# Performance work log

Measured on AMD Instinct MI355X. Metric: run time of the kernel, lower is better.

The kernel has to match this reference:

```python
import jax, jax.numpy as jnp
import numpy as np

S, HID = 2048, 4096
H, KV, D = 32, 8, 128
EPS = 1e-6
THETA = 10000.0


def setup_inputs() -> dict:
    key = jax.random.key(0)
    k0, k1, k2 = jax.random.split(key, 3)
    return {
        "positions": jnp.arange(S, dtype=jnp.int32),
        "hidden_states": jax.random.normal(k0, (S, HID), jnp.float32),
        "w_qkv": jax.random.normal(k1, ((H + 2 * KV) * D, HID), jnp.float32) * 0.02,
        "w_o": jax.random.normal(k2, (HID, H * D), jnp.float32) * 0.02,
        "gq": jnp.ones((D,), jnp.float32),
        "gk": jnp.ones((D,), jnp.float32),
    }


def _rmsnorm(x, g):
    # per-head RMSNorm over last dim (head_dim)
    return x * jax.lax.rsqrt(jnp.mean(x * x, axis=-1, keepdims=True) + EPS) * g


def _rope(x, positions):
    # NeoX-style rotary embedding, rotary_dim == head_dim
    half = D // 2
    inv_freq = 1.0 / (THETA ** (jnp.arange(half, dtype=jnp.float32) * 2.0 / D))
    freqs = positions.astype(jnp.float32)[:, None] * inv_freq  # [S, half]
    cos = jnp.cos(freqs)[:, None, :]  # [S, 1, half]
    sin = jnp.sin(freqs)[:, None, :]
    x1, x2 = x[..., :half], x[..., half:]
    return jnp.concatenate([x1 * cos - x2 * sin, x2 * cos + x1 * sin], axis=-1)


def reference(positions, hidden_states, w_qkv, w_o, gq, gk):
    qkv = hidden_states @ w_qkv.T  # [S, (H+2KV)*D]
    q = qkv[:, : H * D].reshape(S, H, D)
    k = qkv[:, H * D : (H + KV) * D].reshape(S, KV, D)
    v = qkv[:, (H + KV) * D :].reshape(S, KV, D)

    q = _rmsnorm(q, gq)
    k = _rmsnorm(k, gk)
    q = _rope(q, positions)
    k = _rope(k, positions)

    rep = H // KV
    kf = jnp.repeat(k, rep, axis=1)  # [S, H, D]
    vf = jnp.repeat(v, rep, axis=1)

    scale = D ** -0.5
    scores = jnp.einsum("qhd,khd->hqk", q, kf) * scale  # [H, S, S]
    causal = jnp.tril(jnp.ones((S, S), dtype=bool))
    scores = jnp.where(causal[None], scores, jnp.finfo(scores.dtype).min)
    attn = jax.nn.softmax(scores, axis=-1)
    ctx = jnp.einsum("hqk,khd->qhd", attn, vf).reshape(S, H * D)
    return ctx @ w_o.T  # [S, HID]
```

## Files before the change

kernel.cpp:

```cpp
#include <hip/hip_runtime.h>
#include <hip/hip_bf16.h>

#define S_LEN 2048
#define HID   4096
#define NH    32
#define NKV   8
#define DH    128
#define NQKV  ((NH + 2*NKV) * DH)

typedef __attribute__((ext_vector_type(8))) short s16x8;
typedef __attribute__((ext_vector_type(4))) short s16x4;
typedef __attribute__((ext_vector_type(4))) float f32x4;

__device__ __forceinline__ short f2bf(float x) {
    union { __hip_bfloat16 b; short s; } u;
    u.b = __float2bfloat16(x);
    return u.s;
}
__device__ __forceinline__ float bf2f(short s) {
    union { unsigned int u; float f; } v;
    v.u = ((unsigned int)(unsigned short)s) << 16;
    return v.f;
}

__device__ __forceinline__ void gload16(const void* g, void* l) {
    __builtin_amdgcn_global_load_lds(
        (const __attribute__((address_space(1))) void*)g,
        (__attribute__((address_space(3))) void*)l,
        16, 0, 0);
}

__device__ __forceinline__ void cstore(float* p, float v) { *p = v; }
__device__ __forceinline__ void cstore(short* p, float v) { *p = f2bf(v); }

__global__ __launch_bounds__(256) void convert_hs_wqkv(
        const float* __restrict__ in1, short* __restrict__ o1, long n1,
        const float* __restrict__ in2, short* __restrict__ o2, long n2)
{
    const long total = n1 + n2;
    long i0 = ((long)blockIdx.x * blockDim.x + threadIdx.x) * 4;
    long stride = (long)gridDim.x * blockDim.x * 4;
    for (long i = i0; i < total; i += stride) {
        const float* src; short* dst; long off;
        if (i < n1) { src = in1; dst = o1; off = i; }
        else        { src = in2; dst = o2; off = i - n1; }
        float4 v = *(const float4*)(src + off);
        s16x4 o;
        o[0] = f2bf(v.x); o[1] = f2bf(v.y); o[2] = f2bf(v.z); o[3] = f2bf(v.w);
        *(s16x4*)(dst + off) = o;
    }
}

template <typename OT>
__global__ __launch_bounds__(512, 2) void gemm192(
        const short* __restrict__ A, const short* __restrict__ B,
        OT* __restrict__ C, int M, int N, int K)
{
    __shared__ char lds[114688];
    const int t = threadIdx.x;
    const int w = t >> 6, l = t & 63, g = l >> 4, q16 = l & 15;
    const int wm = w >> 2, wn = w & 3;
    const int bx = blockIdx.x, by = blockIdx.y;
    const int NT = K >> 6;

    const int r0 = t >> 3, c0 = t & 7;
    const int scA = c0 ^ (r0 & 7);
    const long KB64  = (long)K * 128;
    const long KB128 = (long)K * 256;
    const long gA00 = ((long)(by * 256 + r0) * K) * 2 + scA * 16;
    long gBoff[3];
#pragma unroll
    for (int i = 0; i < 3; ++i) {
        int row = (i * 512 + t) >> 3;
        int chunk = (t & 7) ^ (row & 7);
        gBoff[i] = ((long)(bx * 192 + row) * K) * 2 + chunk * 16;
    }
    const int dstw = w * 1024;

    auto SA = [&](int kt, int h) {
        char* d = lds + ((kt & 1) * 2 + h) * 16384 + dstw;
        const long s0 = gA00 + h * KB128 + (long)kt * 128;
        gload16((const char*)A + s0, d);
        gload16((const char*)A + s0 + KB64, d + 8192);
    };
    auto SB = [&](int kt) {
        char* d = lds + 65536 + (kt & 1) * 24576 + dstw;
        const long kb = (long)kt * 128;
#pragma unroll
        for (int i = 0; i < 3; ++i)
            gload16((const char*)B + gBoff[i] + kb, d + i * 8192);
    };

    const int arow = q16 * 128;
    const int brow = (wn * 48 + q16) * 128;
    const int sw0 = ((g) ^ (q16 & 7)) << 4;
    const int sw1 = ((4 + g) ^ (q16 & 7)) << 4;

    f32x4 acc[8][3] = {};
    s16x8 a0f[4][2], a1f[4][2], b0f[2][2], b1f[2];

    SB(0); SA(0, 0); SA(0, 1);
    SB(1); SA(1, 0); SA(1, 1);
    asm volatile("s_waitcnt vmcnt(7)" ::: "memory");
    __builtin_amdgcn_s_barrier();

    for (int kt = 0; kt < NT; ++kt) {
        const int b = kt & 1;
        const char* As_ = lds + (b * 2 + wm) * 16384;
        const char* Bs_ = lds + 65536 + b * 24576;

#pragma unroll
        for (int mi = 0; mi < 4; ++mi) {
            a0f[mi][0] = *(const s16x8*)(As_ + arow + mi*2048 + sw0);
            a0f[mi][1] = *(const s16x8*)(As_ + arow + mi*2048 + sw1);
        }
#pragma unroll
        for (int ni = 0; ni < 2; ++ni) {
            b0f[ni][0] = *(const s16x8*)(Bs_ + brow + ni*2048 + sw0);
            b0f[ni][1] = *(const s16x8*)(Bs_ + brow + ni*2048 + sw1);
        }
        __builtin_amdgcn_s_barrier();
        asm volatile("s_waitcnt lgkmcnt(0)" ::: "memory");
        __builtin_amdgcn_sched_barrier(0);
        __builtin_amdgcn_s_setprio(1);
#pragma unroll
        for (int mi = 0; mi < 4; ++mi)
#pragma unroll
            for (int ni = 0; ni < 2; ++ni)
#pragma unroll
                for (int kk = 0; kk < 2; ++kk)
                    acc[mi][ni] = __builtin_amdgcn_mfma_f32_16x16x32_bf16(
                            a0f[mi][kk], b0f[ni][kk], acc[mi][ni], 0, 0, 0);
        __builtin_amdgcn_s_setprio(0);
        __builtin_amdgcn_s_barrier();

        b1f[0] = *(const s16x8*)(Bs_ + brow + 2*2048 + sw0);
        b1f[1] = *(const s16x8*)(Bs_ + brow + 2*2048 + sw1);
#pragma unroll
        for (int mi = 0; mi < 4; ++mi) {
            a1f[mi][0] = *(const s16x8*)(As_ + arow + 8192 + mi*2048 + sw0);
            a1f[mi][1] = *(const s16x8*)(As_ + arow + 8192 + mi*2048 + sw1);
        }
        __builtin_amdgcn_s_barrier();
        asm volatile("s_waitcnt lgkmcnt(0)" ::: "memory");
        __builtin_amdgcn_sched_barrier(0);
        __builtin_amdgcn_s_setprio(1);
#pragma unroll
        for (int mi = 0; mi < 4; ++mi)
#pragma unroll
            for (int kk = 0; kk < 2; ++kk)
                acc[mi][2] = __builtin_amdgcn_mfma_f32_16x16x32_bf16(
                        a0f[mi][kk], b1f[kk], acc[mi][2], 0, 0, 0);
#pragma unroll
        for (int mi = 0; mi < 4; ++mi)
#pragma unroll
            for (int kk = 0; kk < 2; ++kk)
                acc[4+mi][2] = __builtin_amdgcn_mfma_f32_16x16x32_bf16(
                        a1f[mi][kk], b1f[kk], acc[4+mi][2], 0, 0, 0);
        __builtin_amdgcn_s_setprio(0);
        __builtin_amdgcn_s_barrier();

        if (kt + 2 < NT) { SB(kt + 2); SA(kt + 2, 0); SA(kt + 2, 1); }
        __builtin_amdgcn_s_setprio(1);
#pragma unroll
        for (int mi = 0; mi < 4; ++mi)
#pragma unroll
            for (int ni = 0; ni < 2; ++ni)
#pragma unroll
                for (int kk = 0; kk < 2; ++kk)
                    acc[4+mi][ni] = __builtin_amdgcn_mfma_f32_16x16x32_bf16(
                            a1f[mi][kk], b0f[ni][kk], acc[4+mi][ni], 0, 0, 0);
        __builtin_amdgcn_s_setprio(0);
        if (kt + 2 < NT) asm volatile("s_waitcnt vmcnt(7)" ::: "memory");
        else             asm volatile("s_waitcnt vmcnt(0)" ::: "memory");
        __builtin_amdgcn_s_barrier();
    }

#pragma unroll
    for (int mf = 0; mf < 8; ++mf) {
        long row = (long)by * 256 + wm * 128 + mf * 16 + g * 4;
#pragma unroll
        for (int nf = 0; nf < 3; ++nf) {
            long col = (long)bx * 192 + wn * 48 + nf * 16 + q16;
            f32x4 v = acc[mf][nf];
#pragma unroll
            for (int r = 0; r < 4; ++r)
                cstore(&C[(row + r) * (long)N + col], v[r]);
        }
    }
}

template <typename OT>
__global__ __launch_bounds__(512, 4) void gemm_bt(
        const short* __restrict__ A, const short* __restrict__ B,
        OT* __restrict__ C, int M, int N, int K)
{
    __shared__ char lds[64 * 1024];
    const int t = threadIdx.x;
    const int w = t >> 6, l = t & 63, g = l >> 4, q16 = l & 15;
    const int wm = w >> 2, wn = w & 3;
    const long rowA = (long)blockIdx.y * 128;
    const long rowB = (long)blockIdx.x * 128;
    const int NT = K >> 6;

    long goffA[2], goffB[2];
#pragma unroll
    for (int i = 0; i < 2; ++i) {
        int li = i * 512 + t;
        int row = li >> 3;
        int chunk = (t & 7) ^ (row & 7);
        goffA[i] = ((rowA + row) * (long)K) * 2 + chunk * 16;
        goffB[i] = ((rowB + row) * (long)K) * 2 + chunk * 16;
    }
    const int ldsoff = w * 1024;

    int aoff[4][2], boff[2][2];
#pragma unroll
    for (int m = 0; m < 4; ++m)
#pragma unroll
        for (int k = 0; k < 2; ++k) {
            int row = wm * 64 + m * 16 + q16;
            int chunk = (k * 4 + g) ^ (row & 7);
            aoff[m][k] = row * 128 + chunk * 16;
        }
#pragma unroll
    for (int n = 0; n < 2; ++n)
#pragma unroll
        for (int k = 0; k < 2; ++k) {
            int row = wn * 32 + n * 16 + q16;
            int chunk = (k * 4 + g) ^ (row & 7);
            boff[n][k] = row * 128 + chunk * 16;
        }

    auto STAGE = [&](int kt, char* dA, char* dB) {
        const long kb = (long)kt * 128;
#pragma unroll
        for (int i = 0; i < 2; ++i)
            gload16((const char*)A + goffA[i] + kb, dA + i * 8192 + ldsoff);
#pragma unroll
        for (int i = 0; i < 2; ++i)
            gload16((const char*)B + goffB[i] + kb, dB + i * 8192 + ldsoff);
    };

    f32x4 acc[4][2] = {};

    STAGE(0, lds, lds + 32768);
    STAGE(1, lds + 16384, lds + 49152);

    for (int kt = 0; kt < NT; ++kt) {
        const int b = kt & 1;
        char* bA = lds + (b ? 16384 : 0);
        char* bB = lds + (b ? 49152 : 32768);
        if (kt + 1 < NT) asm volatile("s_waitcnt vmcnt(4)" ::: "memory");
        else             asm volatile("s_waitcnt vmcnt(0)" ::: "memory");
        __builtin_amdgcn_s_barrier();

        s16x8 af[4][2], bfr[2][2];
#pragma unroll
        for (int m = 0; m < 4; ++m)
#pragma unroll
            for (int k = 0; k < 2; ++k)
                af[m][k] = *(const s16x8*)(bA + aoff[m][k]);
#pragma unroll
        for (int n = 0; n < 2; ++n)
#pragma unroll
            for (int k = 0; k < 2; ++k)
                bfr[n][k] = *(const s16x8*)(bB + boff[n][k]);

        __builtin_amdgcn_s_setprio(1);
#pragma unroll
        for (int m = 0; m < 4; ++m)
#pragma unroll
            for (int n = 0; n < 2; ++n)
#pragma unroll
                for (int k = 0; k < 2; ++k)
                    acc[m][n] = __builtin_amdgcn_mfma_f32_16x16x32_bf16(
                            af[m][k], bfr[n][k], acc[m][n], 0, 0, 0);
        __builtin_amdgcn_s_setprio(0);
        __builtin_amdgcn_s_barrier();

        if (kt + 2 < NT) STAGE(kt + 2, bA, bB);
    }

#pragma unroll
    for (int m = 0; m < 4; ++m) {
        long row = rowA + wm * 64 + m * 16 + g * 4;
#pragma unroll
        for (int n = 0; n < 2; ++n) {
            long col = rowB + wn * 32 + n * 16 + q16;
            f32x4 v = acc[m][n];
#pragma unroll
            for (int r = 0; r < 4; ++r)
                cstore(&C[(row + r) * (long)N + col], v[r]);
        }
    }
}

__global__ __launch_bounds__(256) void post_gemm1_fused(
        const float* __restrict__ wo, short* __restrict__ wob,
        const short* __restrict__ qkvb, const int* __restrict__ pos,
        const float* __restrict__ gq, const float* __restrict__ gk,
        short* __restrict__ qo, short* __restrict__ ko,
        short* __restrict__ vt)
{
    const int bid = blockIdx.x;

    if (bid < 2048) {
        const long n = (long)HID * (NH * DH);
        long i0 = ((long)bid * 256 + threadIdx.x) * 4;
        long stride = 2048L * 256 * 4;
        for (long i = i0; i < n; i += stride) {
            float4 v = *(const float4*)(wo + i);
            s16x4 o;
            o[0] = f2bf(v.x); o[1] = f2bf(v.y); o[2] = f2bf(v.z); o[3] = f2bf(v.w);
            *(s16x4*)(wob + i) = o;
        }
        return;
    }

    if (bid < 12288) {
        const int idx = bid - 2048;
        const int s = idx / 5;
        const int slot = (idx % 5) * 8 + (threadIdx.x >> 5);
        const int p = threadIdx.x & 31, d = p * 4;

        s16x4 xv = *(const s16x4*)(qkvb + (long)s * NQKV + slot * DH + d);
        float x[4];
#pragma unroll
        for (int r = 0; r < 4; ++r) x[r] = bf2f(xv[r]);

        float ss = x[0]*x[0] + x[1]*x[1] + x[2]*x[2] + x[3]*x[3];
#pragma unroll
        for (int o = 1; o < 32; o <<= 1) ss += __shfl_xor(ss, o);
        float rms = rsqrtf(ss * (1.0f / DH) + 1e-6f);

        const bool isq = slot < NH;
        const float* gp = isq ? gq : gk;
        float y[4];
#pragma unroll
        for (int r = 0; r < 4; ++r) y[r] = x[r] * rms * gp[d + r];

        float y2[4];
#pragma unroll
        for (int r = 0; r < 4; ++r) y2[r] = __shfl_xor(y[r], 16);

        const float po = (float)pos[s];
        const int jbase = d & 63;
        s16x4 ov;
#pragma unroll
        for (int r = 0; r < 4; ++r) {
            float invf = exp2f(-(float)(jbase + r) * (13.287712379549449f / 64.0f));
            float ang = po * invf;
            float c = cosf(ang), sn = sinf(ang);
            float outv = (d < 64) ? (y[r] * c - y2[r] * sn)
                                  : (y[r] * c + y2[r] * sn);
            ov[r] = f2bf(outv);
        }
        if (isq) *(s16x4*)(qo + ((long)s * NH + slot) * DH + d) = ov;
        else     *(s16x4*)(ko + ((long)s * NKV + (slot - NH)) * DH + d) = ov;
        return;
    }

    __shared__ short tile[64][72];
    const int idx2 = bid - 12288;
    const int sb = idx2 & 31, db = (idx2 >> 5) & 1, h = idx2 >> 6;
    const int t = threadIdx.x;
#pragma unroll
    for (int i = 0; i < 2; ++i) {
        int c = i * 256 + t;
        int row = c >> 3, dc = (c & 7) * 8;
        const short* src = qkvb + (long)(sb*64 + row) * NQKV
                           + (NH + NKV + h) * DH + db*64 + dc;
        s16x8 x = *(const s16x8*)src;
#pragma unroll
        for (int jj = 0; jj < 8; ++jj) tile[row][dc + jj] = x[jj];
    }
    __syncthreads();
#pragma unroll
    for (int i = 0; i < 2; ++i) {
        int c = i * 256 + t;
        int dr = c >> 3, sc = (c & 7) * 8;
        s16x8 y;
#pragma unroll
        for (int jj = 0; jj < 8; ++jj) y[jj] = tile[sc + jj][dr];
        short* dst = vt + (long)(h*DH + db*64 + dr) * S_LEN + sb*64 + sc;
        *(s16x8*)dst = y;
    }
}

__device__ __forceinline__ void stage_kv(const char* kgB, const char* vgB,
                                         int kt, int t, char* kd, char* vd)
{
    const int w = t >> 6;
#pragma unroll
    for (int ci = 0; ci < 4; ++ci) {
        int c = ci * 256 + t;
        int row = c >> 4, col16 = c & 15;
        const char* gk = kgB + (long)(kt*64 + row) * (NKV*DH*2)
                         + ((col16*16) ^ ((row & 7) << 4));
        gload16(gk, kd + ci*4096 + w*1024);
        int rowv = c >> 3, scol8 = c & 7;
        const char* gv = vgB + (long)rowv * (S_LEN*2) + kt*128
                         + ((scol8*16) ^ ((rowv & 7) << 4));
        gload16(gv, vd + ci*4096 + w*1024);
    }
}

__global__ __launch_bounds__(256, 2) void attn_kernel(
        const short* __restrict__ qg, const short* __restrict__ kg,
        const short* __restrict__ vtg, short* __restrict__ ctx)
{
    const int bx = blockIdx.x;
    const int h  = bx & 31;
    const int slot = bx >> 5;
    const int qb = (slot < 8) ? slot : 23 - slot;
    const int kvh = h >> 2;
    const int t = threadIdx.x, w = t >> 6, l = t & 63, g = l >> 4, q16 = l & 15;

    __shared__ char Kl[2][16384];
    __shared__ char Vl[2][16384];
    __shared__ short Pl[4][32 * 64];

    const float scale = 0.08838834764831845f;
    const char* kgB = (const char*)kg + (long)kvh * DH * 2;
    const char* vgB = (const char*)vtg + (long)kvh * DH * (long)S_LEN * 2;

    const int nt = 2 * qb + 2;
    int qrow[2];
    qrow[0] = qb*128 + w*32 + q16;
    qrow[1] = qrow[0] + 16;

    s16x8 qf[2][4];
#pragma unroll
    for (int s = 0; s < 2; ++s) {
        const short* qptr = qg + ((long)qrow[s] * NH + h) * DH;
#pragma unroll
        for (int dk = 0; dk < 4; ++dk)
            qf[s][dk] = *(const s16x8*)(qptr + dk*32 + g*8);
    }

    f32x4 oacc[2][8] = {};
    float m_run[2] = {-1e30f, -1e30f}, l_run[2] = {0.f, 0.f};

    stage_kv(kgB, vgB, 0, t, Kl[0], Vl[0]);
    __syncthreads();

    for (int kt = 0; kt < nt; ++kt) {
        const int b = kt & 1;
        if (kt + 1 < nt)
            stage_kv(kgB, vgB, kt + 1, t, Kl[b ^ 1], Vl[b ^ 1]);
        const char* kb = Kl[b];
        const char* vbb = Vl[b];

        f32x4 sacc[2][4] = {};
        __builtin_amdgcn_s_setprio(1);
#pragma unroll
        for (int m = 0; m < 4; ++m) {
            int kvr = m*16 + q16;
            s16x8 af[4];
#pragma unroll
            for (int dk = 0; dk < 4; ++dk) {
                int byte = (kvr*256 + (dk*32 + g*8)*2) ^ ((kvr & 7) << 4);
                af[dk] = *(const s16x8*)(kb + byte);
            }
#pragma unroll
            for (int s = 0; s < 2; ++s)
#pragma unroll
                for (int dk = 0; dk < 4; ++dk)
                    sacc[s][m] = __builtin_amdgcn_mfma_f32_16x16x32_bf16(
                            af[dk], qf[s][dk], sacc[s][m], 0,0,0);
        }
        __builtin_amdgcn_s_setprio(0);

        const bool diag = (kt >= 2*qb);
        float mx[2];
#pragma unroll
        for (int s = 0; s < 2; ++s) {
            mx[s] = -1e30f;
#pragma unroll
            for (int m = 0; m < 4; ++m)
#pragma unroll
                for (int r = 0; r < 4; ++r) {
                    float x = sacc[s][m][r] * scale;
                    if (diag) {
                        int kv = kt*64 + m*16 + g*4 + r;
                        if (kv > qrow[s]) x = -1e30f;
                    }
                    sacc[s][m][r] = x;
                    mx[s] = fmaxf(mx[s], x);
                }
            mx[s] = fmaxf(mx[s], __shfl_xor(mx[s], 16));
            mx[s] = fmaxf(mx[s], __shfl_xor(mx[s], 32));
        }
        if (__any((mx[0] > m_run[0] + 8.f) || (mx[1] > m_run[1] + 8.f))) {
#pragma unroll
            for (int s = 0; s < 2; ++s) {
                float m_new = fmaxf(m_run[s], mx[s]);
                float corr = __expf(m_run[s] - m_new);
                l_run[s] *= corr;
                m_run[s] = m_new;
                float rf[4];
#pragma unroll
                for (int r = 0; r < 4; ++r)
                    rf[r] = __shfl(corr, (g << 4) | (g*4 + r));
#pragma unroll
                for (int nf = 0; nf < 8; ++nf)
#pragma unroll
                    for (int r = 0; r < 4; ++r) oacc[s][nf][r] *= rf[r];
            }
        }
#pragma unroll
        for (int s = 0; s < 2; ++s) {
            float psum = 0.f;
#pragma unroll
            for (int m = 0; m < 4; ++m) {
                s16x4 pk;
#pragma unroll
                for (int r = 0; r < 4; ++r) {
                    float e = __expf(sacc[s][m][r] - m_run[s]);
                    psum += e;
                    pk[r] = f2bf(e);
                }
                int byte = ((s*16 + q16)*128 + (m*16 + g*4)*2) ^ ((q16 & 7) << 4);
                *(s16x4*)((char*)&Pl[w][0] + byte) = pk;
            }
            psum += __shfl_xor(psum, 16);
            psum += __shfl_xor(psum, 32);
            l_run[s] += psum;
        }

        __builtin_amdgcn_s_setprio(1);
#pragma unroll
        for (int ks = 0; ks < 2; ++ks) {
            s16x8 pa[2];
#pragma unroll
            for (int s = 0; s < 2; ++s) {
                int pbyte = ((s*16 + q16)*128 + (ks*32 + g*8)*2) ^ ((q16 & 7) << 4);
                pa[s] = *(const s16x8*)((const char*)&Pl[w][0] + pbyte);
            }
#pragma unroll
            for (int nf = 0; nf < 8; ++nf) {
                int drow = nf*16 + q16;
                int vbyte = (drow*128 + (ks*32 + g*8)*2) ^ ((drow & 7) << 4);
                s16x8 vbf = *(const s16x8*)(vbb + vbyte);
#pragma unroll
                for (int s = 0; s < 2; ++s)
                    oacc[s][nf] = __builtin_amdgcn_mfma_f32_16x16x32_bf16(
                            pa[s], vbf, oacc[s][nf], 0,0,0);
            }
        }
        __builtin_amdgcn_s_setprio(0);
        __syncthreads();
    }

#pragma unroll
    for (int s = 0; s < 2; ++s) {
        float lr[4];
#pragma unroll
        for (int r = 0; r < 4; ++r)
            lr[r] = __shfl(l_run[s], (g << 4) | (g*4 + r));
#pragma unroll
        for (int nf = 0; nf < 8; ++nf)
#pragma unroll
            for (int r = 0; r < 4; ++r) {
                int row = qb*128 + w*32 + s*16 + g*4 + r;
                int col = h*DH + nf*16 + q16;
                float val = oacc[s][nf][r] / lr[r];
                ctx[(long)row * (NH*DH) + col] = f2bf(val);
            }
    }
}

extern "C" void kernel_launch(void* const* d_in, const int* in_sizes, int n_in,
                              void* d_out, int out_size, void* d_ws, size_t ws_size,
                              hipStream_t stream)
{
    const int*   positions = (const int*)  d_in[0];
    const float* hs        = (const float*)d_in[1];
    const float* wqkv      = (const float*)d_in[2];
    const float* wo        = (const float*)d_in[3];
    const float* gq        = (const float*)d_in[4];
    const float* gk        = (const float*)d_in[5];
    float* out = (float*)d_out;
    char* ws = (char*)d_ws;

    const size_t MB = 1ull << 20;
    short* hsb   = (short*)(ws);
    short* ctxb  = (short*)(ws);
    short* wqkvb = (short*)(ws + 16*MB);
    short* wob   = (short*)(ws + 16*MB);
    short* vtbuf = (short*)(ws + 48*MB);
    short* qkvb  = (short*)(ws + 67*MB);
    short* qbuf  = (short*)(ws + 91*MB);
    short* kbuf  = (short*)(ws + 107*MB);

    (void)in_sizes; (void)n_in; (void)out_size; (void)ws_size;

    convert_hs_wqkv<<<2048, 256, 0, stream>>>(
            hs, hsb, (long)S_LEN * HID,
            wqkv, wqkvb, (long)NQKV * HID);
    gemm192<short><<<dim3(NQKV/192, S_LEN/256), 512, 0, stream>>>(
            hsb, wqkvb, qkvb, S_LEN, NQKV, HID);
    post_gemm1_fused<<<12800, 256, 0, stream>>>(
            wo, wob, qkvb, positions, gq, gk, qbuf, kbuf, vtbuf);
    attn_kernel<<<dim3(512), 256, 0, stream>>>(qbuf, kbuf, vtbuf, ctxb);
    gemm_bt<float><<<dim3(HID/128, S_LEN/128), 512, 0, stream>>>(
            ctxb, wob, out, S_LEN, HID, HID);
}
```

Before: 306.4 us.

## Software-pipeline LDS fragment loads across k-tiles with ping-pong B registers

Restructures the GEMM main loop so the next tile's A and B fragments are read from LDS while the current tile's second half of MFMAs runs. B fragments are double-buffered in registers (even/odd sets) and the loop is unrolled by two via a macro. This cuts the barriers per iteration and overlaps ds_read latency with MFMA issue. The cost is higher register pressure and a loop that assumes an even tile count.

New measurement: 302.0 us. No clear change (-1.5%).

```diff
diff --git a/kernel.cpp b/kernel.cpp
--- a/kernel.cpp
+++ b/kernel.cpp
@@ -97,84 +97,90 @@
     const int sw1 = ((4 + g) ^ (q16 & 7)) << 4;
 
     f32x4 acc[8][3] = {};
-    s16x8 a0f[4][2], a1f[4][2], b0f[2][2], b1f[2];
+    s16x8 a0f[4][2], a1f[4][2], bfE[3][2], bfO[3][2];
 
     SB(0); SA(0, 0); SA(0, 1);
     SB(1); SA(1, 0); SA(1, 1);
     asm volatile("s_waitcnt vmcnt(7)" ::: "memory");
     __builtin_amdgcn_s_barrier();
-
-    for (int kt = 0; kt < NT; ++kt) {
-        const int b = kt & 1;
-        const char* As_ = lds + (b * 2 + wm) * 16384;
-        const char* Bs_ = lds + 65536 + b * 24576;
-
+    asm volatile("" ::: "memory");
+    {
+        const char* As_ = lds + wm * 16384;
+        const char* Bs_ = lds + 65536;
 #pragma unroll
         for (int mi = 0; mi < 4; ++mi) {
             a0f[mi][0] = *(const s16x8*)(As_ + arow + mi*2048 + sw0);
             a0f[mi][1] = *(const s16x8*)(As_ + arow + mi*2048 + sw1);
         }
 #pragma unroll
-        for (int ni = 0; ni < 2; ++ni) {
-            b0f[ni][0] = *(const s16x8*)(Bs_ + brow + ni*2048 + sw0);
-            b0f[ni][1] = *(const s16x8*)(Bs_ + brow + ni*2048 + sw1);
-        }
-        __builtin_amdgcn_s_barrier();
-        asm volatile("s_waitcnt lgkmcnt(0)" ::: "memory");
-        __builtin_amdgcn_sched_barrier(0);
-        __builtin_amdgcn_s_setprio(1);
-#pragma unroll
-        for (int mi = 0; mi < 4; ++mi)
-#pragma unroll
-            for (int ni = 0; ni < 2; ++ni)
-#pragma unroll
-                for (int kk = 0; kk < 2; ++kk)
-                    acc[mi][ni] = __builtin_amdgcn_mfma_f32_16x16x32_bf16(
-                            a0f[mi][kk], b0f[ni][kk], acc[mi][ni], 0, 0, 0);
-        __builtin_amdgcn_s_setprio(0);
-        __builtin_amdgcn_s_barrier();
-
-        b1f[0] = *(const s16x8*)(Bs_ + brow + 2*2048 + sw0);
-        b1f[1] = *(const s16x8*)(Bs_ + brow + 2*2048 + sw1);
-#pragma unroll
-        for (int mi = 0; mi < 4; ++mi) {
-            a1f[mi][0] = *(const s16x8*)(As_ + arow + 8192 + mi*2048 + sw0);
-            a1f[mi][1] = *(const s16x8*)(As_ + arow + 8192 + mi*2048 + sw1);
-        }
-        __builtin_amdgcn_s_barrier();
-        asm volatile("s_waitcnt lgkmcnt(0)" ::: "memory");
-        __builtin_amdgcn_sched_barrier(0);
-        __builtin_amdgcn_s_setprio(1);
-#pragma unroll
-        for (int mi = 0; mi < 4; ++mi)
-#pragma unroll
-            for (int kk = 0; kk < 2; ++kk)
-                acc[mi][2] = __builtin_amdgcn_mfma_f32_16x16x32_bf16(
-                        a0f[mi][kk], b1f[kk], acc[mi][2], 0, 0, 0);
-#pragma unroll
-        for (int mi = 0; mi < 4; ++mi)
-#pragma unroll
-            for (int kk = 0; kk < 2; ++kk)
-                acc[4+mi][2] = __builtin_amdgcn_mfma_f32_16x16x32_bf16(
-                        a1f[mi][kk], b1f[kk], acc[4+mi][2], 0, 0, 0);
-        __builtin_amdgcn_s_setprio(0);
-        __builtin_amdgcn_s_barrier();
-
-        if (kt + 2 < NT) { SB(kt + 2); SA(kt + 2, 0); SA(kt + 2, 1); }
-        __builtin_amdgcn_s_setprio(1);
-#pragma unroll
-        for (int mi = 0; mi < 4; ++mi)
-#pragma unroll
-            for (int ni = 0; ni < 2; ++ni)
-#pragma unroll
-                for (int kk = 0; kk < 2; ++kk)
-                    acc[4+mi][ni] = __builtin_amdgcn_mfma_f32_16x16x32_bf16(
-                            a1f[mi][kk], b0f[ni][kk], acc[4+mi][ni], 0, 0, 0);
-        __builtin_amdgcn_s_setprio(0);
-        if (kt + 2 < NT) asm volatile("s_waitcnt vmcnt(7)" ::: "memory");
-        else             asm volatile("s_waitcnt vmcnt(0)" ::: "memory");
-        __builtin_amdgcn_s_barrier();
-    }
+        for (int ni = 0; ni < 3; ++ni) {
+            bfE[ni][0] = *(const s16x8*)(Bs_ + brow + ni*2048 + sw0);
+            bfE[ni][1] = *(const s16x8*)(Bs_ + brow + ni*2048 + sw1);
+        }
+    }
+
+#define GBODY(KT, BCUR, BNXT, PAR) do {                                       \
+    const char* As_ = lds + ((PAR)*2 + wm) * 16384;                           \
+                                  \
+    _Pragma("unroll")                                                         \
+    for (int mi = 0; mi < 4; ++mi) {                                          \
+        a1f[mi][0] = *(const s16x8*)(As_ + arow + 8192 + mi*2048 + sw0);      \
+        a1f[mi][1] = *(const s16x8*)(As_ + arow + 8192 + mi*2048 + sw1);      \
+    }                                                                         \
+    asm volatile("s_waitcnt lgkmcnt(8)" ::: "memory");        \
+    __builtin_amdgcn_sched_barrier(0);                                        \
+    __builtin_amdgcn_s_setprio(1);                                            \
+    _Pragma("unroll")                                                         \
+    for (int mi = 0; mi < 4; ++mi)                                            \
+    _Pragma("unroll")                                                         \
+    for (int ni = 0; ni < 3; ++ni)                                            \
+    _Pragma("unroll")                                                         \
+    for (int kk = 0; kk < 2; ++kk)                                            \
+        acc[mi][ni] = __builtin_amdgcn_mfma_f32_16x16x32_bf16(                \
+                a0f[mi][kk], BCUR[ni][kk], acc[mi][ni], 0, 0, 0);             \
+    __builtin_amdgcn_s_setprio(0);                                            \
+    asm volatile("s_waitcnt lgkmcnt(0)" ::: "memory");        \
+    __builtin_amdgcn_sched_barrier(0);                                        \
+    __builtin_amdgcn_s_barrier();          \
+    if ((KT) + 2 < NT) {                                                      \
+        SB((KT) + 2); SA((KT) + 2, 0); SA((KT) + 2, 1);                       \
+        asm volatile("s_waitcnt vmcnt(7)" ::: "memory");     \
+    } else {                                                                  \
+        asm volatile("s_waitcnt vmcnt(0)" ::: "memory");                      \
+    }                                                                         \
+    __builtin_amdgcn_s_barrier();               \
+    asm volatile("" ::: "memory");                                            \
+    if ((KT) + 1 < NT) {                    \
+        const char* An_ = lds + (((PAR) ^ 1) * 2 + wm) * 16384;               \
+        const char* Bn_ = lds + 65536 + ((PAR) ^ 1) * 24576;                  \
+        _Pragma("unroll")                                                     \
+        for (int mi = 0; mi < 4; ++mi) {                                      \
+            a0f[mi][0] = *(const s16x8*)(An_ + arow + mi*2048 + sw0);         \
+            a0f[mi][1] = *(const s16x8*)(An_ + arow + mi*2048 + sw1);         \
+        }                                                                     \
+        _Pragma("unroll")                                                     \
+        for (int ni = 0; ni < 3; ++ni) {                                      \
+            BNXT[ni][0] = *(const s16x8*)(Bn_ + brow + ni*2048 + sw0);        \
+            BNXT[ni][1] = *(const s16x8*)(Bn_ + brow + ni*2048 + sw1);        \
+        }                                                                     \
+    }                                                                         \
+    __builtin_amdgcn_s_setprio(1);         \
+    _Pragma("unroll")                                                         \
+    for (int mi = 0; mi < 4; ++mi)                                            \
+    _Pragma("unroll")                                                         \
+    for (int ni = 0; ni < 3; ++ni)                                            \
+    _Pragma("unroll")                                                         \
+    for (int kk = 0; kk < 2; ++kk)                                            \
+        acc[4+mi][ni] = __builtin_amdgcn_mfma_f32_16x16x32_bf16(              \
+                a1f[mi][kk], BCUR[ni][kk], acc[4+mi][ni], 0, 0, 0);           \
+    __builtin_amdgcn_s_setprio(0);                                            \
+} while (0)
+
+    for (int kt = 0; kt < NT; kt += 2) {
+        GBODY(kt,     bfE, bfO, 0);
+        GBODY(kt + 1, bfO, bfE, 1);
+    }
+#undef GBODY
 
 #pragma unroll
     for (int mf = 0; mf < 8; ++mf) {
```
